# Optimization experiments

Hardware: AMD Instinct MI355X
Metric: run time of the kernel (lower is better)

Reference implementation:

```python
import jax, jax.numpy as jnp
import numpy as np
import math

V, T, E, N = 32000, 128, 64, 1024
SIGMA_MIN, SIGMA_MAX, C = 0.1, 10.0, 2.0


def setup_inputs() -> dict:
    key = jax.random.key(0)
    k1, k2, k3, k4, k5 = jax.random.split(key, 5)
    return {
        "x": jax.random.normal(k1, (T, N), dtype=jnp.float32),
        "mu": jax.random.normal(k2, (V, E), dtype=jnp.float32),
        "log_sigma": jax.random.normal(k3, (V, E), dtype=jnp.float32),
        "mu_c": jax.random.normal(k4, (T, E), dtype=jnp.float32),
        "log_sigma_c": jax.random.normal(k5, (T, E), dtype=jnp.float32),
        "t": 0,
    }


def reference(x, mu, log_sigma, mu_c, log_sigma_c, t):
    # parameter clamping done in-place in the torch forward
    bound = math.sqrt(C)
    mu = jnp.clip(mu, -bound, bound)
    mu_c = jnp.clip(mu_c, -bound, bound)
    log_sigma = jnp.clip(log_sigma, math.log(SIGMA_MIN), math.log(SIGMA_MAX))
    log_sigma_c = jnp.clip(log_sigma_c, math.log(SIGMA_MIN), math.log(SIGMA_MAX))

    sigma = jnp.exp(log_sigma)        # [V, E]
    sigma_c = jnp.exp(log_sigma_c)    # [T, E]

    # pairwise Gaussian expected-likelihood energy, vectorized over topics
    s = sigma[:, None, :] + sigma_c[None, :, :]            # [V, T, E]
    det_fac = jnp.sum(jnp.log(s), axis=-1)                 # [V, T]
    diff = mu[:, None, :] - mu_c[None, :, :]               # [V, T, E]
    diff_mu = jnp.sum(diff * diff / s, axis=-1)            # [V, T]
    emb_dim = mu.shape[-1]
    log_el = -0.5 * (det_fac + diff_mu + emb_dim * math.log(2.0 * math.pi))

    # per-topic softmax over the vocab axis
    w = jax.nn.softmax(log_el, axis=0)                     # [V, T]

    return w @ x.reshape(-1, x.shape[-1])                  # [V, N]
```

## Files before the change

kernel.cpp:

```cpp
#include <hip/hip_runtime.h>
#include <math.h>

#define VV 32000
#define TT 128
#define EE 64
#define NN 1024
#define NPART 500

static constexpr float BOUND    = 1.41421356237309515f;
static constexpr float LOG_SMIN = -2.30258509299404568f;
static constexpr float LOG_SMAX =  2.30258509299404568f;
static constexpr float LN2      =  0.69314718055994531f;
static constexpr float LOG2E    =  1.44269504088896340f;
static constexpr float E_LOG2PI =  64.0f * 1.83787706640934548f;

typedef __attribute__((ext_vector_type(2)))  float f32x2;
typedef __attribute__((ext_vector_type(8)))  short short8;
typedef __attribute__((ext_vector_type(16))) float float16;

static __device__ inline unsigned short f2bf(float f) {
    union { float f; unsigned u; } v; v.f = f;
    unsigned r = v.u + 0x7FFFu + ((v.u >> 16) & 1u);
    return (unsigned short)(r >> 16);
}

static __device__ inline unsigned pack_bf16(float a, float b) {
    unsigned r;
    asm("v_cvt_pk_bf16_f32 %0, %1, %2" : "=v"(r) : "v"(a), "v"(b));
    return r;
}

__global__ __launch_bounds__(256) void prep_xpose(const float* __restrict__ mu_c,
                                                  const float* __restrict__ log_sigma_c,
                                                  const float* __restrict__ x,
                                                  float* __restrict__ sc,
                                                  float* __restrict__ mc,
                                                  unsigned short* __restrict__ xT) {
    const int tid = threadIdx.x;
    if (blockIdx.x < 32) {
        int i = blockIdx.x * 256 + tid;
        if (i < TT * EE) {
            float ls = log_sigma_c[i];
            ls = fminf(fmaxf(ls, LOG_SMIN), LOG_SMAX);
            sc[i] = __expf(ls);
            float m = mu_c[i];
            mc[i] = fminf(fmaxf(m, -BOUND), BOUND);
        }
    } else {
        const int b = blockIdx.x - 32;
        const int n = b * 32 + (tid & 31);
        const int th = tid >> 5;
        const float* __restrict__ xp = x + n;
#pragma unroll
        for (int i = 0; i < 16; i += 2) {
            int t = th * 16 + i;
            float x0 = xp[(size_t)t * NN];
            float x1 = xp[(size_t)(t + 1) * NN];
            *(unsigned*)&xT[n * TT + t] = (unsigned)f2bf(x0) | ((unsigned)f2bf(x1) << 16);
        }
    }
}

__global__ __launch_bounds__(256) void logits_kernel(const float* __restrict__ mu,
                                                     const float* __restrict__ log_sigma,
                                                     const float* __restrict__ sc,
                                                     const float* __restrict__ mc,
                                                     float* __restrict__ logitsT,
                                                     float* __restrict__ pm,
                                                     float* __restrict__ pl) {
    __shared__ float part[16][4][64];
    const int tid  = threadIdx.x;
    const int lane = tid & 63;
    const int wv   = tid >> 6;
    const int v0   = blockIdx.x * 64;
    const int t0   = blockIdx.y * 32;
    const int e0u  = __builtin_amdgcn_readfirstlane(wv) * 16;

    f32x2 sv[8], mv[8];
    {
        const float* __restrict__ lsp = log_sigma + (size_t)(v0 + lane) * EE + e0u;
        const float* __restrict__ mup = mu        + (size_t)(v0 + lane) * EE + e0u;
#pragma unroll
        for (int j = 0; j < 8; j++) {
            float a = lsp[2 * j], b = lsp[2 * j + 1];
            a = fminf(fmaxf(a, LOG_SMIN), LOG_SMAX);
            b = fminf(fmaxf(b, LOG_SMIN), LOG_SMAX);
            sv[j] = f32x2{__expf(a), __expf(b)};
            float c = mup[2 * j], d = mup[2 * j + 1];
            mv[j] = f32x2{fminf(fmaxf(c, -BOUND), BOUND), fminf(fmaxf(d, -BOUND), BOUND)};
        }
    }

    f32x2 cs[2][8], cm[2][8];
    {
        const f32x2* __restrict__ sp = (const f32x2*)(sc + t0 * EE + e0u);
        const f32x2* __restrict__ mp = (const f32x2*)(mc + t0 * EE + e0u);
#pragma unroll
        for (int j = 0; j < 8; j++) { cs[0][j] = sp[j]; cm[0][j] = mp[j]; }
    }

    for (int tb = 0; tb < 2; tb++) {
#pragma unroll
        for (int i = 0; i < 16; i++) {
            const int ti  = tb * 16 + i;
            const int cur = ti & 1;
            if (ti < 31) {
                const int tn = t0 + ti + 1;
                const f32x2* __restrict__ sp = (const f32x2*)(sc + tn * EE + e0u);
                const f32x2* __restrict__ mp = (const f32x2*)(mc + tn * EE + e0u);
#pragma unroll
                for (int j = 0; j < 8; j++) { cs[cur ^ 1][j] = sp[j]; cm[cur ^ 1][j] = mp[j]; }
            }
            f32x2 q = {0.f, 0.f};
            f32x2 p = {1.f, 1.f};
#pragma unroll
            for (int j = 0; j < 8; j++) {
                f32x2 s = sv[j] + cs[cur][j];
                p *= s;
                f32x2 d = mv[j] - cm[cur][j];
                f32x2 r;
                r.x = __builtin_amdgcn_rcpf(s.x);
                r.y = __builtin_amdgcn_rcpf(s.y);
                q += d * d * r;
            }
            part[i][wv][lane] = __log2f(p.x * p.y) * LN2 + q.x + q.y;
        }
        __syncthreads();
#pragma unroll
        for (int k = 0; k < 4; k++) {
            const int i = wv * 4 + k;
            const int t = t0 + tb * 16 + i;
            float sum = part[i][0][lane] + part[i][1][lane] + part[i][2][lane] + part[i][3][lane];
            float logit = -0.5f * (sum + E_LOG2PI);
            logitsT[t * VV + v0 + lane] = logit;

            float m = logit;
#pragma unroll
            for (int off = 1; off < 64; off <<= 1) m = fmaxf(m, __shfl_xor(m, off));
            float sx = __expf(logit - m);
#pragma unroll
            for (int off = 1; off < 64; off <<= 1) sx += __shfl_xor(sx, off);
            if (lane == 0) {
                pm[t * NPART + blockIdx.x] = m;
                pl[t * NPART + blockIdx.x] = sx;
            }
        }
        __syncthreads();
    }
}

__global__ __launch_bounds__(256) void merge_stats(const float* __restrict__ pm,
                                                   const float* __restrict__ pl,
                                                   float* __restrict__ stats) {
    const int tid = threadIdx.x;
    const int t = blockIdx.x;
    __shared__ float red[8];
    float m = -3.4e38f;
    for (int j = tid; j < NPART; j += 256) m = fmaxf(m, pm[t * NPART + j]);
#pragma unroll
    for (int off = 1; off < 64; off <<= 1) m = fmaxf(m, __shfl_xor(m, off));
    if ((tid & 63) == 0) red[tid >> 6] = m;
    __syncthreads();
    m = fmaxf(fmaxf(red[0], red[1]), fmaxf(red[2], red[3]));

    float l = 0.0f;
    for (int j = tid; j < NPART; j += 256)
        l += pl[t * NPART + j] * __expf(pm[t * NPART + j] - m);
#pragma unroll
    for (int off = 1; off < 64; off <<= 1) l += __shfl_xor(l, off);
    if ((tid & 63) == 0) red[4 + (tid >> 6)] = l;
    __syncthreads();
    if (tid == 0) {
        float tot = red[4] + red[5] + red[6] + red[7];
        stats[t] = -(__log2f(tot) + m * LOG2E);
    }
}

__global__ __launch_bounds__(256) void wx_mfma(const float* __restrict__ logitsT,
                                               const float* __restrict__ stats,
                                               const unsigned short* __restrict__ xT,
                                               float* __restrict__ out) {
    const int tid = threadIdx.x;
    const int n0 = blockIdx.x * 128;
    const int v0 = blockIdx.y * 64;
    const int lane = tid & 63;
    const int wv   = tid >> 6;
    const int vh   = (wv & 1) * 32;
    const int nh   = (wv >> 1) * 64;
    const int r32  = lane & 31;
    const int koff = (lane >> 5) * 8;

    const float* __restrict__ lp = logitsT + (size_t)koff * VV + v0 + vh + r32;
    const float* __restrict__ cp = stats + koff;
    const unsigned short* __restrict__ bp0 = xT + (size_t)(n0 + nh + r32) * TT + koff;
    const unsigned short* __restrict__ bp1 = bp0 + 32 * TT;

    float16 acc0 = {0,0,0,0,0,0,0,0,0,0,0,0,0,0,0,0};
    float16 acc1 = {0,0,0,0,0,0,0,0,0,0,0,0,0,0,0,0};
#pragma unroll 2
    for (int kb = 0; kb < 8; kb++) {
        float lg[8], c[8];
#pragma unroll
        for (int j = 0; j < 8; j++) {
            lg[j] = lp[(size_t)(kb * 16 + j) * VV];
            c[j]  = cp[kb * 16 + j];
        }
        union { short8 v; unsigned u[4]; } a;
#pragma unroll
        for (int j = 0; j < 4; j++) {
            float w0 = exp2f(fmaf(lg[2 * j],     LOG2E, c[2 * j]));
            float w1 = exp2f(fmaf(lg[2 * j + 1], LOG2E, c[2 * j + 1]));
            a.u[j] = pack_bf16(w0, w1);
        }
        short8 b0 = *(const short8*)(bp0 + kb * 16);
        short8 b1 = *(const short8*)(bp1 + kb * 16);
        acc0 = __builtin_amdgcn_mfma_f32_32x32x16_bf16(a.v, b0, acc0, 0, 0, 0);
        acc1 = __builtin_amdgcn_mfma_f32_32x32x16_bf16(a.v, b1, acc1, 0, 0, 0);
    }

    const int col = lane & 31;
    const int rbase = 4 * (lane >> 5);
#pragma unroll
    for (int r = 0; r < 16; r++) {
        int row = (r & 3) + 8 * (r >> 2) + rbase;
        float* dst = out + (size_t)(v0 + vh + row) * NN + n0 + nh + col;
        dst[0]  = acc0[r];
        dst[32] = acc1[r];
    }
}

extern "C" void kernel_launch(void* const* d_in, const int* in_sizes, int n_in,
                              void* d_out, int out_size, void* d_ws, size_t ws_size,
                              hipStream_t stream) {
    const float* x           = (const float*)d_in[0];
    const float* mu          = (const float*)d_in[1];
    const float* log_sigma   = (const float*)d_in[2];
    const float* mu_c        = (const float*)d_in[3];
    const float* log_sigma_c = (const float*)d_in[4];
    float* out = (float*)d_out;

    float* ws      = (float*)d_ws;
    float* logitsT = ws;
    float* pm      = logitsT + (size_t)TT * VV;
    float* pl      = pm + (size_t)TT * NPART;
    float* stats   = pl + (size_t)TT * NPART;
    float* sc      = stats + TT;
    float* mc      = sc + TT * EE;
    unsigned short* xT = (unsigned short*)(mc + TT * EE);

    prep_xpose<<<64, 256, 0, stream>>>(mu_c, log_sigma_c, x, sc, mc, xT);
    logits_kernel<<<dim3(VV / 64, 4), 256, 0, stream>>>(mu, log_sigma, sc, mc,
                                                        logitsT, pm, pl);
    merge_stats<<<TT, 256, 0, stream>>>(pm, pl, stats);
    wx_mfma<<<dim3(NN / 128, VV / 64), 256, 0, stream>>>(logitsT, stats, xT, out);
}
```

Measured before the change: 257.7 us.

## Store logits V-major via LDS transpose and remap GEMM blocks for locality

The logits kernel now stages its per-block logits in shared memory and writes them V-major ([V][T]) with float4 stores. This lets the GEMM kernel read each row's 16 K-values as contiguous float4 loads instead of strided scalar loads across rows of length V. The GEMM grid becomes 1D with a swizzled block-to-tile mapping, presumably to group blocks for cache locality across XCDs. The loop is fully unrolled. The cost is extra LDS use and a sync-free transpose step, plus 96 idle blocks that exit immediately in the padded grid.

```diff
diff --git a/kernel.cpp b/kernel.cpp
--- a/kernel.cpp
+++ b/kernel.cpp
@@ -65,10 +65,11 @@
                                                      const float* __restrict__ log_sigma,
                                                      const float* __restrict__ sc,
                                                      const float* __restrict__ mc,
-                                                     float* __restrict__ logitsT,
+                                                     float* __restrict__ logitsVT,
                                                      float* __restrict__ pm,
                                                      float* __restrict__ pl) {
     __shared__ float part[16][4][64];
+    __shared__ float lvt[64][33];
     const int tid  = threadIdx.x;
     const int lane = tid & 63;
     const int wv   = tid >> 6;
@@ -132,7 +133,7 @@
             const int t = t0 + tb * 16 + i;
             float sum = part[i][0][lane] + part[i][1][lane] + part[i][2][lane] + part[i][3][lane];
             float logit = -0.5f * (sum + E_LOG2PI);
-            logitsT[t * VV + v0 + lane] = logit;
+            lvt[lane][tb * 16 + i] = logit;
 
             float m = logit;
 #pragma unroll
@@ -146,6 +147,19 @@
             }
         }
         __syncthreads();
+    }
+
+    {
+        const int v  = tid >> 2;
+        const int c0 = (tid & 3) * 8;
+        float4 d0, d1;
+        d0.x = lvt[v][c0 + 0]; d0.y = lvt[v][c0 + 1];
+        d0.z = lvt[v][c0 + 2]; d0.w = lvt[v][c0 + 3];
+        d1.x = lvt[v][c0 + 4]; d1.y = lvt[v][c0 + 5];
+        d1.z = lvt[v][c0 + 6]; d1.w = lvt[v][c0 + 7];
+        float* dst = logitsVT + (size_t)(v0 + v) * TT + t0 + c0;
+        *(float4*)dst       = d0;
+        *(float4*)(dst + 4) = d1;
     }
 }
 
@@ -176,13 +190,20 @@
     }
 }
 
-__global__ __launch_bounds__(256) void wx_mfma(const float* __restrict__ logitsT,
+__global__ __launch_bounds__(256) void wx_mfma(const float* __restrict__ logitsVT,
                                                const float* __restrict__ stats,
                                                const unsigned short* __restrict__ xT,
                                                float* __restrict__ out) {
+    const int g  = blockIdx.x;
+    const int x8 = g & 7;
+    const int k  = g >> 3;
+    const int vt = x8 * 64 + (k >> 3);
+    const int nc = k & 7;
+    if (vt >= VV / 64) return;
+
     const int tid = threadIdx.x;
-    const int n0 = blockIdx.x * 128;
-    const int v0 = blockIdx.y * 64;
+    const int n0 = nc * 128;
+    const int v0 = vt * 64;
     const int lane = tid & 63;
     const int wv   = tid >> 6;
     const int vh   = (wv & 1) * 32;
@@ -190,28 +211,27 @@
     const int r32  = lane & 31;
     const int koff = (lane >> 5) * 8;
 
-    const float* __restrict__ lp = logitsT + (size_t)koff * VV + v0 + vh + r32;
+    const float* __restrict__ lp = logitsVT + (size_t)(v0 + vh + r32) * TT + koff;
     const float* __restrict__ cp = stats + koff;
     const unsigned short* __restrict__ bp0 = xT + (size_t)(n0 + nh + r32) * TT + koff;
     const unsigned short* __restrict__ bp1 = bp0 + 32 * TT;
 
     float16 acc0 = {0,0,0,0,0,0,0,0,0,0,0,0,0,0,0,0};
     float16 acc1 = {0,0,0,0,0,0,0,0,0,0,0,0,0,0,0,0};
-#pragma unroll 2
+#pragma unroll
     for (int kb = 0; kb < 8; kb++) {
-        float lg[8], c[8];
-#pragma unroll
-        for (int j = 0; j < 8; j++) {
-            lg[j] = lp[(size_t)(kb * 16 + j) * VV];
-            c[j]  = cp[kb * 16 + j];
-        }
+        float4 l0 = *(const float4*)(lp + kb * 16);
+        float4 l1 = *(const float4*)(lp + kb * 16 + 4);
+        float c[8];
+#pragma unroll
+        for (int j = 0; j < 8; j++) c[j] = cp[kb * 16 + j];
+
         union { short8 v; unsigned u[4]; } a;
-#pragma unroll
-        for (int j = 0; j < 4; j++) {
-            float w0 = exp2f(fmaf(lg[2 * j],     LOG2E, c[2 * j]));
-            float w1 = exp2f(fmaf(lg[2 * j + 1], LOG2E, c[2 * j + 1]));
-            a.u[j] = pack_bf16(w0, w1);
-        }
+        a.u[0] = pack_bf16(exp2f(fmaf(l0.x, LOG2E, c[0])), exp2f(fmaf(l0.y, LOG2E, c[1])));
+        a.u[1] = pack_bf16(exp2f(fmaf(l0.z, LOG2E, c[2])), exp2f(fmaf(l0.w, LOG2E, c[3])));
+        a.u[2] = pack_bf16(exp2f(fmaf(l1.x, LOG2E, c[4])), exp2f(fmaf(l1.y, LOG2E, c[5])));
+        a.u[3] = pack_bf16(exp2f(fmaf(l1.z, LOG2E, c[6])), exp2f(fmaf(l1.w, LOG2E, c[7])));
+
         short8 b0 = *(const short8*)(bp0 + kb * 16);
         short8 b1 = *(const short8*)(bp1 + kb * 16);
         acc0 = __builtin_amdgcn_mfma_f32_32x32x16_bf16(a.v, b0, acc0, 0, 0, 0);
@@ -239,18 +259,18 @@
     const float* log_sigma_c = (const float*)d_in[4];
     float* out = (float*)d_out;
 
-    float* ws      = (float*)d_ws;
-    float* logitsT = ws;
-    float* pm      = logitsT + (size_t)TT * VV;
-    float* pl      = pm + (size_t)TT * NPART;
-    float* stats   = pl + (size_t)TT * NPART;
-    float* sc      = stats + TT;
-    float* mc      = sc + TT * EE;
+    float* ws       = (float*)d_ws;
+    float* logitsVT = ws;
+    float* pm       = logitsVT + (size_t)TT * VV;
+    float* pl       = pm + (size_t)TT * NPART;
+    float* stats    = pl + (size_t)TT * NPART;
+    float* sc       = stats + TT;
+    float* mc       = sc + TT * EE;
     unsigned short* xT = (unsigned short*)(mc + TT * EE);
 
     prep_xpose<<<64, 256, 0, stream>>>(mu_c, log_sigma_c, x, sc, mc, xT);
     logits_kernel<<<dim3(VV / 64, 4), 256, 0, stream>>>(mu, log_sigma, sc, mc,
-                                                        logitsT, pm, pl);
+                                                        logitsVT, pm, pl);
     merge_stats<<<TT, 256, 0, stream>>>(pm, pl, stats);
-    wx_mfma<<<dim3(NN / 128, VV / 64), 256, 0, stream>>>(logitsT, stats, xT, out);
-}
+    wx_mfma<<<4096, 256, 0, stream>>>(logitsVT, stats, xT, out);
+}
```

Result: no change. 254.3 us (-1.3%).
